# Optimization experiments

Hardware: AMD Instinct MI355X
Metric: run time of the kernel (lower is better)

Reference implementation:

```python
import jax, jax.numpy as jnp
import numpy as np

V = 50000      # vocab size
FEAT = 300     # glove dim
HID = 512      # num_hidden
C = 20         # class_num (GAT feature width)
L = 2          # num_layers
NH = 4         # num_heads
K = 3          # diffusion hops
ALPHA = 0.1    # teleport prob
N = 76800      # total nodes in batched graph
E = 1250000    # total edges
B = 512        # number of graphs (docs)
SLOPE = 0.2    # leaky relu slope (DGL GAT default)


def setup_inputs() -> dict:
    key = jax.random.key(0)
    ks = jax.random.split(key, 12)
    node_ids = jax.random.randint(ks[0], (N,), 0, V)
    edge_src = jax.random.randint(ks[1], (E,), 0, N)
    edge_dst = jax.random.randint(ks[2], (E,), 0, N)
    graph_ids = jnp.sort(jax.random.randint(ks[3], (N,), 0, B))
    emb = jax.random.uniform(ks[4], (V, FEAT), minval=-0.1, maxval=0.1, dtype=jnp.float32)
    W1 = jax.random.normal(ks[5], (FEAT, HID), dtype=jnp.float32) / np.sqrt(FEAT)
    b1 = jnp.zeros((HID,), jnp.float32)
    W2 = jax.random.normal(ks[6], (HID, C), dtype=jnp.float32) / np.sqrt(HID)
    b2 = jnp.zeros((C,), jnp.float32)
    gat_W = jax.random.normal(ks[7], (L, NH, C, C), dtype=jnp.float32) / np.sqrt(C)
    gat_asrc = jax.random.normal(ks[8], (L, NH, C), dtype=jnp.float32) * 0.1
    gat_adst = jax.random.normal(ks[9], (L, NH, C), dtype=jnp.float32) * 0.1
    ws_W = jax.random.normal(ks[10], (C, 1), dtype=jnp.float32) / np.sqrt(C)
    ws_b = jnp.zeros((1,), jnp.float32)
    return {"node_ids": node_ids, "edge_src": edge_src, "edge_dst": edge_dst,
            "graph_ids": graph_ids, "emb": emb, "W1": W1, "b1": b1, "W2": W2,
            "b2": b2, "gat_W": gat_W, "gat_asrc": gat_asrc, "gat_adst": gat_adst,
            "ws_W": ws_W, "ws_b": ws_b}


def _segment_softmax(e, dst, n):
    # e: [NH, E] edge scores; softmax over edges sharing the same destination node
    seg_max = jax.vmap(lambda v: jax.ops.segment_max(v, dst, num_segments=n))(e)
    seg_max = jnp.where(jnp.isfinite(seg_max), seg_max, 0.0)
    ex = jnp.exp(e - seg_max[:, dst])
    denom = jax.vmap(lambda v: jax.ops.segment_sum(v, dst, num_segments=n))(ex)
    return ex / (denom[:, dst] + 1e-9)


def _forward(node_ids, edge_src, edge_dst, graph_ids, emb, W1, b1, W2, b2,
             gat_W, gat_asrc, gat_adst, ws_W, ws_b):
    x = jnp.take(emb, node_ids, axis=0)              # [N, FEAT] embedding lookup
    x = jax.nn.relu(x @ W1 + b1)                     # [N, HID]
    h = x @ W2 + b2                                  # [N, C]
    for l in range(L):
        z = jnp.einsum('nc,hcd->hnd', h, gat_W[l])   # [NH, N, C]
        es = jnp.einsum('hnd,hd->hn', z, gat_asrc[l])
        ed = jnp.einsum('hnd,hd->hn', z, gat_adst[l])
        e = jax.nn.leaky_relu(es[:, edge_src] + ed[:, edge_dst], SLOPE)  # [NH, E]
        att = _segment_softmax(e, edge_dst, N)       # [NH, E]
        # attention diffusion: H <- (1-alpha) * A_att @ H + alpha * H0
        H0 = z
        Hc = z
        for _ in range(K):
            msg = att[:, :, None] * Hc[:, edge_src, :]                     # [NH, E, C]
            agg = jax.vmap(lambda m: jax.ops.segment_sum(m, edge_dst, num_segments=N))(msg)
            Hc = (1.0 - ALPHA) * agg + ALPHA * H0
        h = Hc.mean(axis=0)                          # merge='mean' over heads
        if l < L - 1:
            h = jax.nn.elu(h)
    gate = jax.nn.sigmoid(h @ ws_W + ws_b)           # [N, 1] WeightAndSum gate
    return jax.ops.segment_sum(h * gate, graph_ids, num_segments=B)  # [B, C]


def reference(node_ids, edge_src, edge_dst, graph_ids, emb, W1, b1, W2, b2,
              gat_W, gat_asrc, gat_adst, ws_W, ws_b):
    return _forward(node_ids, edge_src, edge_dst, graph_ids, emb, W1, b1, W2, b2,
                    gat_W, gat_asrc, gat_adst, ws_W, ws_b)
```

## Files before the change

kernel.cpp:

```cpp
#include <hip/hip_runtime.h>
#include <hip/hip_bf16.h>
#include <hip/hip_fp16.h>
#include <math.h>

#define VOCAB 50000
#define FEAT 300
#define KPAD 320
#define HID 512
#define C 20
#define NL 2
#define NH 4
#define KHOP 3
#define ALPHA 0.1f
#define NNODE 76800
#define NEDGE 1250000
#define NB 512
#define SLOPE 0.2f

#define NBKT 300
#define BKTCAP 5120
#define NSLOT (NBKT * BKTCAP)
#define EPB 5120
#define NEBLK ((NEDGE + EPB - 1) / EPB)

#define BM 32
#define VPAD 50048
#define SX_STRIDE 520
#define WSTRIDE 21

typedef float f32x4 __attribute__((ext_vector_type(4)));
typedef short bf16x8 __attribute__((ext_vector_type(8)));

__device__ inline unsigned short f2b(float x) {
  __hip_bfloat16 h = __float2bfloat16(x);
  return *reinterpret_cast<unsigned short*>(&h);
}

union R20 {
  struct { uint4 a, b; uint2 c; } v;
  __half2 h[10];
};
__device__ inline R20 ldrow20(const __half* p) {
  R20 r;
  r.v.a = *(const uint4*)p;
  r.v.b = *(const uint4*)(p + 8);
  r.v.c = *(const uint2*)(p + 16);
  return r;
}
__device__ inline void strow20(__half* p, const R20& r) {
  *(uint4*)p = r.v.a;
  *(uint4*)(p + 8) = r.v.b;
  *(uint2*)(p + 16) = r.v.c;
}

#define H2SWZ(v, pat) ({ union { __half2 h; int i; } _u; _u.h = (v);          \
                         _u.i = __builtin_amdgcn_ds_swizzle(_u.i, (pat));     \
                         _u.h; })
#define FSWZ(x, pat) __int_as_float(                                          \
    __builtin_amdgcn_ds_swizzle(__float_as_int(x), (pat)))
#define SLOTRED_H2(v) do {                                                    \
    v = __hadd2(v, H2SWZ(v, 0x101F));                                         \
    v = __hadd2(v, H2SWZ(v, 0x201F));                                         \
    v = __hadd2(v, H2SWZ(v, 0x401F)); } while (0)

__global__ void k_cvt_w1(const float* __restrict__ W1, ushort* __restrict__ W1t)
{
  int idx = blockIdx.x * 256 + threadIdx.x;
  int kc = idx >> 12;
  int rem = idx & 4095;
  int col = rem >> 3;
  int j = rem & 7;
  int k = kc * 8 + j;
  W1t[idx] = (k < FEAT) ? f2b(W1[(size_t)k * HID + col]) : (ushort)0;
}

__global__ void k_prep_coef(const float* __restrict__ gatW0,
                            const float* __restrict__ as0,
                            const float* __restrict__ ad0,
                            const float* __restrict__ b2,
                            float* __restrict__ coef, float* __restrict__ bb)
{
  int col = threadIdx.x;
  if (col >= 96) return;
  float cf[C];
  if (col < 80) {
    int hd = col / C, d = col - hd * C;
#pragma unroll
    for (int j = 0; j < C; j++) cf[j] = gatW0[(hd * C + j) * C + d];
  } else if (col < 88) {
    int hd = col - 80;
#pragma unroll
    for (int j = 0; j < C; j++) {
      float s = 0.f;
#pragma unroll
      for (int d = 0; d < C; d++) s += gatW0[(hd * C + j) * C + d] * as0[hd * C + d];
      cf[j] = s;
    }
  } else {
    int hd = col - 88;
#pragma unroll
    for (int j = 0; j < C; j++) {
      float s = 0.f;
#pragma unroll
      for (int d = 0; d < C; d++) s += gatW0[(hd * C + j) * C + d] * ad0[hd * C + d];
      cf[j] = s;
    }
  }
  float bbv = 0.f;
#pragma unroll
  for (int j = 0; j < C; j++) { coef[col * C + j] = cf[j]; bbv += b2[j] * cf[j]; }
  bb[col] = bbv;
}

__global__ void k_prep_wcp(const float* __restrict__ W2,
                           const float* __restrict__ coef,
                           ushort* __restrict__ Wcpt)
{
  int idx = blockIdx.x * 256 + threadIdx.x;
  int kc = idx / 768;
  int rem = idx - kc * 768;
  int col = rem >> 3;
  int j = rem & 7;
  int k = kc * 8 + j;
  float s = 0.f;
#pragma unroll
  for (int jj = 0; jj < C; jj++) s += W2[(size_t)k * C + jj] * coef[col * C + jj];
  Wcpt[idx] = f2b(s);
}

__global__ __launch_bounds__(512, 6) void k_mlp_mfma(
    const float* __restrict__ emb, const ushort* __restrict__ W1t,
    const float* __restrict__ b1, const ushort* __restrict__ Wcpt,
    const float* __restrict__ bb, __half* __restrict__ zfull,
    float* __restrict__ esf, float* __restrict__ edf)
{
  __shared__ ushort smem[16640];
  ushort* sA = smem;
  ushort* sX = smem;

  const int t = threadIdx.x;
  const int lane = t & 63;
  const int w = t >> 6;
  const int v0 = blockIdx.x * BM;
  const int l15 = lane & 15;
  const int l4 = lane >> 4;
  const int cb = w * 64;

#pragma unroll
  for (int j = 0; j < 3; j++) {
    int chunk = j * 512 + t;
    if (chunk < 1280) {
      int row = chunk & 31;
      int kc = chunk >> 5;
      int vr = v0 + row;
      if (vr >= VOCAB) vr = VOCAB - 1;
      int k0 = kc * 8;
      const float* p = emb + (size_t)vr * FEAT + k0;
      ushort u[8];
      if (k0 + 8 <= FEAT) {
        float4 x = *(const float4*)p;
        float4 y = *(const float4*)(p + 4);
        u[0] = f2b(x.x); u[1] = f2b(x.y); u[2] = f2b(x.z); u[3] = f2b(x.w);
        u[4] = f2b(y.x); u[5] = f2b(y.y); u[6] = f2b(y.z); u[7] = f2b(y.w);
      } else {
#pragma unroll
        for (int q = 0; q < 8; q++)
          u[q] = (k0 + q < FEAT) ? f2b(p[q]) : (ushort)0;
      }
      *(uint4*)(sA + (size_t)chunk * 8) = *(const uint4*)u;
    }
  }
  __syncthreads();

  f32x4 acc[2][4];
#pragma unroll
  for (int rt = 0; rt < 2; rt++)
#pragma unroll
    for (int ct = 0; ct < 4; ct++) acc[rt][ct] = (f32x4)0.f;

  for (int ks = 0; ks < 10; ks++) {
    const int kcb = ks * 4 + l4;
    bf16x8 a0 = *(const bf16x8*)(sA + ((size_t)kcb * 32 + l15) * 8);
    bf16x8 a1 = *(const bf16x8*)(sA + ((size_t)kcb * 32 + 16 + l15) * 8);
    const ushort* wb = W1t + ((size_t)kcb * 512 + cb + l15) * 8;
    bf16x8 bf[4];
#pragma unroll
    for (int ct = 0; ct < 4; ct++) bf[ct] = *(const bf16x8*)(wb + ct * 128);
#pragma unroll
    for (int ct = 0; ct < 4; ct++) {
      acc[0][ct] = __builtin_amdgcn_mfma_f32_16x16x32_bf16(a0, bf[ct], acc[0][ct], 0, 0, 0);
      acc[1][ct] = __builtin_amdgcn_mfma_f32_16x16x32_bf16(a1, bf[ct], acc[1][ct], 0, 0, 0);
    }
  }
  __syncthreads();

#pragma unroll
  for (int rt = 0; rt < 2; rt++)
#pragma unroll
    for (int ct = 0; ct < 4; ct++) {
      int col = cb + ct * 16 + l15;
      float bias = b1[col];
#pragma unroll
      for (int r4 = 0; r4 < 4; r4++) {
        int row = rt * 16 + l4 * 4 + r4;
        float x = fmaxf(acc[rt][ct][r4] + bias, 0.f);
        sX[(size_t)row * SX_STRIDE + col] = f2b(x);
      }
    }
  __syncthreads();

  const int ntile = (w < 4) ? 2 : 1;
  for (int i = 0; i < ntile; i++) {
    const int tt = (i == 0) ? w : 8 + w;
    const int rt = tt & 1, ct = tt >> 1;
    const ushort* xb = sX + (size_t)(rt * 16 + l15) * SX_STRIDE + l4 * 8;
    const ushort* wbp = Wcpt + ((size_t)l4 * 96 + ct * 16 + l15) * 8;
    bf16x8 bv[16];
#pragma unroll
    for (int ks = 0; ks < 16; ks++)
      bv[ks] = *(const bf16x8*)(wbp + (size_t)ks * 3072);
    f32x4 a2 = (f32x4)0.f;
#pragma unroll
    for (int ks = 0; ks < 16; ks++) {
      bf16x8 av = *(const bf16x8*)(xb + ks * 32);
      a2 = __builtin_amdgcn_mfma_f32_16x16x32_bf16(av, bv[ks], a2, 0, 0, 0);
    }
    const int col = ct * 16 + l15;
    const float bias = bb[col];
#pragma unroll
    for (int r = 0; r < 4; r++) {
      const int vrow = v0 + rt * 16 + l4 * 4 + r;
      if (vrow >= VOCAB) continue;
      float val = a2[r] + bias;
      if (col < 80) {
        int hd = col / C, c = col - hd * C;
        zfull[((size_t)vrow * NH + hd) * 20 + c] = __float2half_rn(val);
      } else if (col < 88) {
        esf[(size_t)vrow * NH + (col - 80)] = val;
      } else {
        edf[(size_t)vrow * NH + (col - 88)] = val;
      }
    }
  }
}

__global__ __launch_bounds__(256) void k_bkt_scatter(
    const int* __restrict__ src, const int* __restrict__ dst,
    int* __restrict__ gcur, int* __restrict__ gbuf)
{
  __shared__ int hist[NBKT];
  __shared__ int lcur[NBKT];
  const int t = threadIdx.x;
  for (int i = t; i < NBKT; i += 256) hist[i] = 0;
  __syncthreads();
  const int base = blockIdx.x * EPB;
#pragma unroll
  for (int j = 0; j < 20; j++) {
    int e = base + j * 256 + t;
    if (e < NEDGE) atomicAdd(&hist[dst[e] >> 8], 1);
  }
  __syncthreads();
  for (int i = t; i < NBKT; i += 256) {
    int v = hist[i];
    lcur[i] = v ? atomicAdd(&gcur[i], v) : 0;
  }
  __syncthreads();
#pragma unroll
  for (int j = 0; j < 20; j++) {
    int e = base + j * 256 + t;
    if (e < NEDGE) {
      int d = dst[e];
      int b = d >> 8;
      int idx = atomicAdd(&lcur[b], 1);
      if (idx < BKTCAP)
        gbuf[(size_t)b * BKTCAP + idx] = (src[e] << 8) | (d & 255);
    }
  }
}

__global__ __launch_bounds__(256) void k_csr_build(
    const int* __restrict__ gcur, const int* __restrict__ gbuf,
    const int* __restrict__ node_ids, int* __restrict__ offs,
    int* __restrict__ deg, int* __restrict__ srcc, int* __restrict__ srcv)
{
  __shared__ int shist[256];
  __shared__ int lcur[256];
  __shared__ int wsum[4];
  const int b = blockIdx.x;
  const int t = threadIdx.x;
  const int base = b * BKTCAP;
  int nb = gcur[b];
  if (nb > BKTCAP) nb = BKTCAP;
  shist[t] = 0;
  __syncthreads();
  for (int i = t; i < nb; i += 256)
    atomicAdd(&shist[gbuf[base + i] & 255], 1);
  __syncthreads();
  int v = shist[t];
  int x = v;
#pragma unroll
  for (int off = 1; off < 64; off <<= 1) {
    int y = __shfl_up(x, off, 64);
    if ((t & 63) >= off) x += y;
  }
  if ((t & 63) == 63) wsum[t >> 6] = x;
  __syncthreads();
  int waveoff = 0;
#pragma unroll
  for (int w = 0; w < 4; w++) waveoff += (w < (t >> 6)) ? wsum[w] : 0;
  int pre = base + waveoff + x - v;
  offs[b * 256 + t] = pre;
  deg[b * 256 + t] = v;
  lcur[t] = pre;
  __syncthreads();
  for (int i = t; i < nb; i += 256) {
    int p = gbuf[base + i];
    int slot = atomicAdd(&lcur[p & 255], 1);
    int s = p >> 8;
    srcc[slot] = s;
    srcv[slot] = node_ids[s];
  }
}

__global__ __launch_bounds__(256) void k_hop_first(
    const int* __restrict__ offs, const int* __restrict__ deg,
    const int* __restrict__ sidx,
    const float* __restrict__ esT, const float* __restrict__ edT,
    const int* __restrict__ ids, const __half* __restrict__ Zt,
    __half* __restrict__ att, float* __restrict__ invden,
    __half* __restrict__ Hout)
{
  const int t = threadIdx.x;
  const int head = t & 3;
  const int eslot = (t >> 2) & 7;
  const int n = blockIdx.x * 8 + (t >> 5);
  const int g = n * NH + head;
  const int idn = ids ? ids[n] : n;
  const int beg = offs[n], end = beg + deg[n];
  const float edv = edT[(size_t)idn * NH + head];
  R20 h0 = ldrow20(Zt + ((size_t)idn * NH + head) * 20);
  __half2 agg[10];
#pragma unroll
  for (int q = 0; q < 10; q++) agg[q] = __floats2half2_rn(0.f, 0.f);
  float den = 0.f;
  int p = beg + eslot;
  while (p + 8 < end) {
    int sv0 = sidx[p];
    int sv1 = sidx[p + 8];
    float es0 = esT[(size_t)sv0 * NH + head];
    float es1 = esT[(size_t)sv1 * NH + head];
    R20 r0 = ldrow20(Zt + ((size_t)sv0 * NH + head) * 20);
    R20 r1 = ldrow20(Zt + ((size_t)sv1 * NH + head) * 20);
    float e0 = es0 + edv; e0 = e0 > 0.f ? e0 : SLOPE * e0;
    float e1 = es1 + edv; e1 = e1 > 0.f ? e1 : SLOPE * e1;
    float ex0 = __expf(e0), ex1 = __expf(e1);
    att[(size_t)p * NH + head] = __float2half_rn(ex0);
    att[(size_t)(p + 8) * NH + head] = __float2half_rn(ex1);
    den += ex0 + ex1;
    __half2 a0 = __float2half2_rn(ex0);
    __half2 a1 = __float2half2_rn(ex1);
#pragma unroll
    for (int q = 0; q < 10; q++) {
      agg[q] = __hfma2(a0, r0.h[q], agg[q]);
      agg[q] = __hfma2(a1, r1.h[q], agg[q]);
    }
    p += 16;
  }
  if (p < end) {
    int sv0 = sidx[p];
    float es0 = esT[(size_t)sv0 * NH + head];
    R20 r0 = ldrow20(Zt + ((size_t)sv0 * NH + head) * 20);
    float e0 = es0 + edv; e0 = e0 > 0.f ? e0 : SLOPE * e0;
    float ex0 = __expf(e0);
    att[(size_t)p * NH + head] = __float2half_rn(ex0);
    den += ex0;
    __half2 a0 = __float2half2_rn(ex0);
#pragma unroll
    for (int q = 0; q < 10; q++) agg[q] = __hfma2(a0, r0.h[q], agg[q]);
  }
#pragma unroll
  for (int q = 0; q < 10; q++) SLOTRED_H2(agg[q]);
  den += FSWZ(den, 0x101F);
  den += FSWZ(den, 0x201F);
  den += FSWZ(den, 0x401F);
  if (eslot == 0) {
    float inv = 1.f / (den + 1e-9f);
    invden[g] = inv;
    __half2 s2 = __float2half2_rn(inv * (1.0f - ALPHA));
    __half2 al = __float2half2_rn(ALPHA);
    R20 o;
#pragma unroll
    for (int q = 0; q < 10; q++)
      o.h[q] = __hfma2(s2, agg[q], __hmul2(al, h0.h[q]));
    strow20(Hout + (size_t)g * 20, o);
  }
}

__global__ __launch_bounds__(256) void k_hop_mid(
    const int* __restrict__ offs, const int* __restrict__ deg,
    const int* __restrict__ srcc,
    const __half* __restrict__ att, const float* __restrict__ invden,
    const __half* __restrict__ Hin, const __half* __restrict__ Zt,
    const int* __restrict__ ids, __half* __restrict__ Hout)
{
  const int t = threadIdx.x;
  const int head = t & 3;
  const int eslot = (t >> 2) & 7;
  const int n = blockIdx.x * 8 + (t >> 5);
  const int g = n * NH + head;
  const int idn = ids ? ids[n] : n;
  const int beg = offs[n], end = beg + deg[n];
  R20 h0 = ldrow20(Zt + ((size_t)idn * NH + head) * 20);
  __half2 agg[10];
#pragma unroll
  for (int q = 0; q < 10; q++) agg[q] = __floats2half2_rn(0.f, 0.f);
  int p = beg + eslot;
  while (p + 8 < end) {
    __half a0h = att[(size_t)p * NH + head];
    __half a1h = att[(size_t)(p + 8) * NH + head];
    int sn0 = srcc[p];
    int sn1 = srcc[p + 8];
    R20 r0 = ldrow20(Hin + ((size_t)sn0 * NH + head) * 20);
    R20 r1 = ldrow20(Hin + ((size_t)sn1 * NH + head) * 20);
    __half2 a0 = __half2half2(a0h);
    __half2 a1 = __half2half2(a1h);
#pragma unroll
    for (int q = 0; q < 10; q++) {
      agg[q] = __hfma2(a0, r0.h[q], agg[q]);
      agg[q] = __hfma2(a1, r1.h[q], agg[q]);
    }
    p += 16;
  }
  if (p < end) {
    __half a0h = att[(size_t)p * NH + head];
    int sn0 = srcc[p];
    R20 r0 = ldrow20(Hin + ((size_t)sn0 * NH + head) * 20);
    __half2 a0 = __half2half2(a0h);
#pragma unroll
    for (int q = 0; q < 10; q++) agg[q] = __hfma2(a0, r0.h[q], agg[q]);
  }
#pragma unroll
  for (int q = 0; q < 10; q++) SLOTRED_H2(agg[q]);
  if (eslot == 0) {
    __half2 s2 = __float2half2_rn(invden[g] * (1.0f - ALPHA));
    __half2 al = __float2half2_rn(ALPHA);
    R20 o;
#pragma unroll
    for (int q = 0; q < 10; q++)
      o.h[q] = __hfma2(s2, agg[q], __hmul2(al, h0.h[q]));
    strow20(Hout + (size_t)g * 20, o);
  }
}

__global__ __launch_bounds__(256) void k_hop_last_proj(
    const int* __restrict__ offs, const int* __restrict__ deg,
    const int* __restrict__ srcc,
    const __half* __restrict__ att, const float* __restrict__ invden,
    const __half* __restrict__ Hin, const __half* __restrict__ Zt,
    const int* __restrict__ ids,
    const float* __restrict__ gatW1, const float* __restrict__ as1,
    const float* __restrict__ ad1,
    __half* __restrict__ zb, float* __restrict__ es, float* __restrict__ ed)
{
  __shared__ float sWt[NH * C * WSTRIDE];
  __shared__ float sa[NH * C], sd[NH * C];
  const int t = threadIdx.x;
  for (int i = t; i < NH * C * C; i += 256) {
    int h = i / (C * C);
    int r = i - h * C * C;
    int c = r / C;
    int d = r - c * C;
    sWt[(h * C + d) * WSTRIDE + c] = gatW1[i];
  }
  if (t < NH * C) { sa[t] = as1[t]; sd[t] = ad1[t]; }
  __syncthreads();

  const int head = t & 3;
  const int eslot = (t >> 2) & 7;
  const int n = blockIdx.x * 8 + (t >> 5);
  const int g = n * NH + head;
  const int idn = ids ? ids[n] : n;
  const int beg = offs[n], end = beg + deg[n];
  R20 h0 = ldrow20(Zt + ((size_t)idn * NH + head) * 20);
  __half2 agg[10];
#pragma unroll
  for (int q = 0; q < 10; q++) agg[q] = __floats2half2_rn(0.f, 0.f);
  int p = beg + eslot;
  while (p + 8 < end) {
    __half a0h = att[(size_t)p * NH + head];
    __half a1h = att[(size_t)(p + 8) * NH + head];
    int sn0 = srcc[p];
    int sn1 = srcc[p + 8];
    R20 r0 = ldrow20(Hin + ((size_t)sn0 * NH + head) * 20);
    R20 r1 = ldrow20(Hin + ((size_t)sn1 * NH + head) * 20);
    __half2 a0 = __half2half2(a0h);
    __half2 a1 = __half2half2(a1h);
#pragma unroll
    for (int q = 0; q < 10; q++) {
      agg[q] = __hfma2(a0, r0.h[q], agg[q]);
      agg[q] = __hfma2(a1, r1.h[q], agg[q]);
    }
    p += 16;
  }
  if (p < end) {
    __half a0h = att[(size_t)p * NH + head];
    int sn0 = srcc[p];
    R20 r0 = ldrow20(Hin + ((size_t)sn0 * NH + head) * 20);
    __half2 a0 = __half2half2(a0h);
#pragma unroll
    for (int q = 0; q < 10; q++) agg[q] = __hfma2(a0, r0.h[q], agg[q]);
  }
#pragma unroll
  for (int q = 0; q < 10; q++) SLOTRED_H2(agg[q]);

  __half2 s2 = __float2half2_rn(invden[g] * (1.0f - ALPHA));
  __half2 al = __float2half2_rn(ALPHA);
  float o[C];
#pragma unroll
  for (int q = 0; q < 10; q++) {
    __half2 m = __hfma2(s2, agg[q], __hmul2(al, h0.h[q]));
    m = __hadd2(m, H2SWZ(m, 0x041F));
    m = __hadd2(m, H2SWZ(m, 0x081F));
    float2 f = __half22float2(m);
    float v0 = f.x * 0.25f, v1 = f.y * 0.25f;
    o[2 * q]     = v0 > 0.f ? v0 : __expf(v0) - 1.f;
    o[2 * q + 1] = v1 > 0.f ? v1 : __expf(v1) - 1.f;
  }

  float esp = 0.f, edp = 0.f;
#pragma unroll
  for (int j = 0; j < 3; j++) {
    int d = eslot + j * 8;
    if (d < C) {
      const float* wrow = &sWt[(head * C + d) * WSTRIDE];
      float zv = 0.f;
#pragma unroll
      for (int c = 0; c < C; c++) zv += o[c] * wrow[c];
      esp += zv * sa[head * C + d];
      edp += zv * sd[head * C + d];
      zb[((size_t)n * NH + head) * 20 + d] = __float2half_rn(zv);
    }
  }
  esp += FSWZ(esp, 0x101F);
  esp += FSWZ(esp, 0x201F);
  esp += FSWZ(esp, 0x401F);
  edp += FSWZ(edp, 0x101F);
  edp += FSWZ(edp, 0x201F);
  edp += FSWZ(edp, 0x401F);
  if (eslot == 0) {
    es[g] = esp;
    ed[g] = edp;
  }
}

#define RSPAN 16
__global__ __launch_bounds__(256) void k_hop_last_final(
    const int* __restrict__ offs, const int* __restrict__ deg,
    const int* __restrict__ srcc,
    const __half* __restrict__ att, const float* __restrict__ invden,
    const __half* __restrict__ Hin, const __half* __restrict__ Zt,
    const int* __restrict__ gids, const float* __restrict__ wsW,
    const float* __restrict__ wsb, float* __restrict__ out)
{
  __shared__ float sacc[RSPAN * C];
  __shared__ int sgmin;
  const int t = threadIdx.x;
  const int head = t & 3;
  const int eslot = (t >> 2) & 7;
  const int n = blockIdx.x * 8 + (t >> 5);
  const int g = n * NH + head;
  const int beg = offs[n], end = beg + deg[n];
  for (int i = t; i < RSPAN * C; i += 256) sacc[i] = 0.f;
  if (t == 0) sgmin = gids[blockIdx.x * 8];
  __syncthreads();
  R20 h0 = ldrow20(Zt + ((size_t)n * NH + head) * 20);
  __half2 agg[10];
#pragma unroll
  for (int q = 0; q < 10; q++) agg[q] = __floats2half2_rn(0.f, 0.f);
  int p = beg + eslot;
  while (p + 8 < end) {
    __half a0h = att[(size_t)p * NH + head];
    __half a1h = att[(size_t)(p + 8) * NH + head];
    int sn0 = srcc[p];
    int sn1 = srcc[p + 8];
    R20 r0 = ldrow20(Hin + ((size_t)sn0 * NH + head) * 20);
    R20 r1 = ldrow20(Hin + ((size_t)sn1 * NH + head) * 20);
    __half2 a0 = __half2half2(a0h);
    __half2 a1 = __half2half2(a1h);
#pragma unroll
    for (int q = 0; q < 10; q++) {
      agg[q] = __hfma2(a0, r0.h[q], agg[q]);
      agg[q] = __hfma2(a1, r1.h[q], agg[q]);
    }
    p += 16;
  }
  if (p < end) {
    __half a0h = att[(size_t)p * NH + head];
    int sn0 = srcc[p];
    R20 r0 = ldrow20(Hin + ((size_t)sn0 * NH + head) * 20);
    __half2 a0 = __half2half2(a0h);
#pragma unroll
    for (int q = 0; q < 10; q++) agg[q] = __hfma2(a0, r0.h[q], agg[q]);
  }
#pragma unroll
  for (int q = 0; q < 10; q++) SLOTRED_H2(agg[q]);
  if (eslot == 0) {
    __half2 s2 = __float2half2_rn(invden[g] * (1.0f - ALPHA));
    __half2 al = __float2half2_rn(ALPHA);
    float o[C];
#pragma unroll
    for (int q = 0; q < 10; q++) {
      __half2 m = __hfma2(s2, agg[q], __hmul2(al, h0.h[q]));
      m = __hadd2(m, H2SWZ(m, 0x041F));
      m = __hadd2(m, H2SWZ(m, 0x081F));
      float2 f = __half22float2(m);
      o[2 * q]     = f.x * 0.25f;
      o[2 * q + 1] = f.y * 0.25f;
    }
    float dotp = 0.f;
#pragma unroll
    for (int j = 0; j < 5; j++) {
      int c = head * 5 + j;
      dotp += o[c] * wsW[c];
    }
    dotp += FSWZ(dotp, 0x041F);
    dotp += FSWZ(dotp, 0x081F);
    const float gate = 1.f / (1.f + __expf(-(dotp + wsb[0])));
    const int b = gids[n];
    const int lb = b - sgmin;
    if (lb < RSPAN) {
#pragma unroll
      for (int j = 0; j < 5; j++) {
        int c = head * 5 + j;
        atomicAdd(&sacc[lb * C + c], o[c] * gate);
      }
    } else {
#pragma unroll
      for (int j = 0; j < 5; j++) {
        int c = head * 5 + j;
        atomicAdd(&out[(size_t)b * C + c], o[c] * gate);
      }
    }
  }
  __syncthreads();
  for (int i = t; i < RSPAN * C; i += 256) {
    float v = sacc[i];
    if (v != 0.f) atomicAdd(&out[(size_t)(sgmin + i / C) * C + (i - (i / C) * C)], v);
  }
}

extern "C" void kernel_launch(void* const* d_in, const int* in_sizes, int n_in,
                              void* d_out, int out_size, void* d_ws, size_t ws_size,
                              hipStream_t stream)
{
  const int*   node_ids = (const int*)  d_in[0];
  const int*   edge_src = (const int*)  d_in[1];
  const int*   edge_dst = (const int*)  d_in[2];
  const int*   graph_ids= (const int*)  d_in[3];
  const float* emb      = (const float*)d_in[4];
  const float* W1       = (const float*)d_in[5];
  const float* b1       = (const float*)d_in[6];
  const float* W2       = (const float*)d_in[7];
  const float* b2       = (const float*)d_in[8];
  const float* gat_W    = (const float*)d_in[9];
  const float* gat_asrc = (const float*)d_in[10];
  const float* gat_adst = (const float*)d_in[11];
  const float* ws_W     = (const float*)d_in[12];
  const float* ws_b     = (const float*)d_in[13];
  float* out = (float*)d_out;

  float* esf    = (float*)d_ws;
  float* edf    = esf   + (size_t)VPAD * NH;
  float* es     = edf   + (size_t)VPAD * NH;
  float* ed     = es    + (size_t)NNODE * NH;
  float* invden = ed    + (size_t)NNODE * NH;
  float* bb     = invden+ (size_t)NNODE * NH;
  float* coef   = bb + 96;
  int*   offs   = (int*)(coef + 96 * C);
  int*   deg    = offs + NNODE;
  int*   gcur   = deg + NNODE;
  int*   srcc   = gcur + NBKT;
  int*   srcv   = srcc + NSLOT;
  uintptr_t a16 = ((uintptr_t)(srcv + NSLOT) + 15) & ~(uintptr_t)15;
  __half* zfull = (__half*)a16;
  __half* zb    = zfull + (size_t)VPAD * NH * 20;
  __half* bufA  = zb    + (size_t)NNODE * NH * 20;
  __half* bufB  = bufA  + (size_t)NNODE * NH * 20;
  ushort* W1t   = (ushort*)(bufB + (size_t)NNODE * NH * 20);
  ushort* Wcpt  = W1t + (size_t)40 * 512 * 8;
  uintptr_t x16 = ((uintptr_t)(Wcpt + 64 * 96 * 8) + 15) & ~(uintptr_t)15;
  int*    gbuf  = (int*)x16;
  __half* att   = (__half*)x16;

  hipMemsetAsync(out, 0, (size_t)NB * C * sizeof(float), stream);
  hipMemsetAsync(gcur, 0, NBKT * sizeof(int), stream);

  k_cvt_w1<<<(40 * 512 * 8) / 256, 256, 0, stream>>>(W1, W1t);
  k_prep_coef<<<1, 128, 0, stream>>>(gat_W, gat_asrc, gat_adst, b2, coef, bb);
  k_prep_wcp<<<(64 * 96 * 8) / 256, 256, 0, stream>>>(W2, coef, Wcpt);

  k_bkt_scatter<<<NEBLK, 256, 0, stream>>>(edge_src, edge_dst, gcur, gbuf);
  k_csr_build<<<NBKT, 256, 0, stream>>>(gcur, gbuf, node_ids,
                                        offs, deg, srcc, srcv);

  k_mlp_mfma<<<VPAD / BM, 512, 0, stream>>>(emb, W1t, b1, Wcpt, bb,
                                            zfull, esf, edf);

  const int HB = NNODE / 8;
  k_hop_first<<<HB, 256, 0, stream>>>(offs, deg, srcv, esf, edf, node_ids,
                                      zfull, att, invden, bufA);
  k_hop_mid<<<HB, 256, 0, stream>>>(offs, deg, srcc, att, invden, bufA, zfull,
                                    node_ids, bufB);
  k_hop_last_proj<<<HB, 256, 0, stream>>>(offs, deg, srcc, att, invden, bufB,
                                          zfull, node_ids,
                                          gat_W + (size_t)NH * C * C,
                                          gat_asrc + NH * C, gat_adst + NH * C,
                                          zb, es, ed);
  k_hop_first<<<HB, 256, 0, stream>>>(offs, deg, srcc, es, ed,
                                      (const int*)nullptr, zb, att, invden,
                                      bufA);
  k_hop_mid<<<HB, 256, 0, stream>>>(offs, deg, srcc, att, invden, bufA, zb,
                                    (const int*)nullptr, bufB);
  k_hop_last_final<<<HB, 256, 0, stream>>>(offs, deg, srcc, att, invden, bufB,
                                           zb, graph_ids, ws_W, ws_b, out);
}
```

Baseline: 398.3 us.

## Pad feature rows to 24 halves and pack attention scores into row

Node feature rows grow from 20 to 24 halves so each row is three aligned 16-byte loads, and the per-node source/destination attention scores are stored as fp16 in the padding slots. Edge gathers now fetch the score together with the feature row instead of from separate float arrays. The MLP kernel also gets explicit double-buffered weight loads and a lower occupancy hint. The trade-off is 20% more bytes per row in the gathered buffers and reduced precision for the attention scores.

```diff
diff --git a/kernel.cpp b/kernel.cpp
--- a/kernel.cpp
+++ b/kernel.cpp
@@ -27,6 +27,7 @@
 #define VPAD 50048
 #define SX_STRIDE 520
 #define WSTRIDE 21
+#define RW 24
 
 typedef float f32x4 __attribute__((ext_vector_type(4)));
 typedef short bf16x8 __attribute__((ext_vector_type(8)));
@@ -36,21 +37,22 @@
   return *reinterpret_cast<unsigned short*>(&h);
 }
 
-union R20 {
-  struct { uint4 a, b; uint2 c; } v;
-  __half2 h[10];
+union R24 {
+  uint4 u[3];
+  __half2 h[12];
+  __half s[24];
 };
-__device__ inline R20 ldrow20(const __half* p) {
-  R20 r;
-  r.v.a = *(const uint4*)p;
-  r.v.b = *(const uint4*)(p + 8);
-  r.v.c = *(const uint2*)(p + 16);
+__device__ inline R24 ldrow24(const __half* p) {
+  R24 r;
+  r.u[0] = *(const uint4*)p;
+  r.u[1] = *(const uint4*)(p + 8);
+  r.u[2] = *(const uint4*)(p + 16);
   return r;
 }
-__device__ inline void strow20(__half* p, const R20& r) {
-  *(uint4*)p = r.v.a;
-  *(uint4*)(p + 8) = r.v.b;
-  *(uint2*)(p + 16) = r.v.c;
+__device__ inline void strow24(__half* p, const R24& r) {
+  *(uint4*)p = r.u[0];
+  *(uint4*)(p + 8) = r.u[1];
+  *(uint4*)(p + 16) = r.u[2];
 }
 
 #define H2SWZ(v, pat) ({ union { __half2 h; int i; } _u; _u.h = (v);          \
@@ -128,11 +130,10 @@
   Wcpt[idx] = f2b(s);
 }
 
-__global__ __launch_bounds__(512, 6) void k_mlp_mfma(
+__global__ __launch_bounds__(512, 4) void k_mlp_mfma(
     const float* __restrict__ emb, const ushort* __restrict__ W1t,
     const float* __restrict__ b1, const ushort* __restrict__ Wcpt,
-    const float* __restrict__ bb, __half* __restrict__ zfull,
-    float* __restrict__ esf, float* __restrict__ edf)
+    const float* __restrict__ bb, __half* __restrict__ zfull)
 {
   __shared__ ushort smem[16640];
   ushort* sA = smem;
@@ -178,19 +179,31 @@
 #pragma unroll
     for (int ct = 0; ct < 4; ct++) acc[rt][ct] = (f32x4)0.f;
 
-  for (int ks = 0; ks < 10; ks++) {
-    const int kcb = ks * 4 + l4;
-    bf16x8 a0 = *(const bf16x8*)(sA + ((size_t)kcb * 32 + l15) * 8);
-    bf16x8 a1 = *(const bf16x8*)(sA + ((size_t)kcb * 32 + 16 + l15) * 8);
-    const ushort* wb = W1t + ((size_t)kcb * 512 + cb + l15) * 8;
-    bf16x8 bf[4];
-#pragma unroll
-    for (int ct = 0; ct < 4; ct++) bf[ct] = *(const bf16x8*)(wb + ct * 128);
-#pragma unroll
-    for (int ct = 0; ct < 4; ct++) {
-      acc[0][ct] = __builtin_amdgcn_mfma_f32_16x16x32_bf16(a0, bf[ct], acc[0][ct], 0, 0, 0);
-      acc[1][ct] = __builtin_amdgcn_mfma_f32_16x16x32_bf16(a1, bf[ct], acc[1][ct], 0, 0, 0);
-    }
+  const ushort* wbase = W1t + ((size_t)l4 * 512 + cb + l15) * 8;
+  bf16x8 bfA[4], bfB[4];
+#define LOADB(DST, KS)                                                        \
+  { _Pragma("unroll")                                                         \
+    for (int ct = 0; ct < 4; ct++)                                            \
+      DST[ct] = *(const bf16x8*)(wbase + (size_t)(KS) * 16384 + ct * 128); }
+#define DOMFMA(BF, KS)                                                        \
+  { const int kcb = (KS) * 4 + l4;                                            \
+    bf16x8 a0 = *(const bf16x8*)(sA + ((size_t)kcb * 32 + l15) * 8);          \
+    bf16x8 a1 = *(const bf16x8*)(sA + ((size_t)kcb * 32 + 16 + l15) * 8);     \
+    _Pragma("unroll")                                                         \
+    for (int ct = 0; ct < 4; ct++) {                                          \
+      acc[0][ct] = __builtin_amdgcn_mfma_f32_16x16x32_bf16(a0, BF[ct],        \
+                                                           acc[0][ct], 0, 0, 0);\
+      acc[1][ct] = __builtin_amdgcn_mfma_f32_16x16x32_bf16(a1, BF[ct],        \
+                                                           acc[1][ct], 0, 0, 0);\
+    } }
+
+  LOADB(bfA, 0);
+#pragma unroll
+  for (int ks2 = 0; ks2 < 10; ks2 += 2) {
+    LOADB(bfB, ks2 + 1);
+    DOMFMA(bfA, ks2);
+    if (ks2 + 2 < 10) LOADB(bfA, ks2 + 2);
+    DOMFMA(bfB, ks2 + 1);
   }
   __syncthreads();
 
@@ -234,11 +247,11 @@
       float val = a2[r] + bias;
       if (col < 80) {
         int hd = col / C, c = col - hd * C;
-        zfull[((size_t)vrow * NH + hd) * 20 + c] = __float2half_rn(val);
+        zfull[((size_t)vrow * NH + hd) * RW + c] = __float2half_rn(val);
       } else if (col < 88) {
-        esf[(size_t)vrow * NH + (col - 80)] = val;
+        zfull[((size_t)vrow * NH + (col - 80)) * RW + 20] = __float2half_rn(val);
       } else {
-        edf[(size_t)vrow * NH + (col - 88)] = val;
+        zfull[((size_t)vrow * NH + (col - 88)) * RW + 21] = __float2half_rn(val);
       }
     }
   }
@@ -325,7 +338,6 @@
 __global__ __launch_bounds__(256) void k_hop_first(
     const int* __restrict__ offs, const int* __restrict__ deg,
     const int* __restrict__ sidx,
-    const float* __restrict__ esT, const float* __restrict__ edT,
     const int* __restrict__ ids, const __half* __restrict__ Zt,
     __half* __restrict__ att, float* __restrict__ invden,
     __half* __restrict__ Hout)
@@ -337,8 +349,8 @@
   const int g = n * NH + head;
   const int idn = ids ? ids[n] : n;
   const int beg = offs[n], end = beg + deg[n];
-  const float edv = edT[(size_t)idn * NH + head];
-  R20 h0 = ldrow20(Zt + ((size_t)idn * NH + head) * 20);
+  R24 h0 = ldrow24(Zt + ((size_t)idn * NH + head) * RW);
+  const float edv = __half2float(h0.s[21]);
   __half2 agg[10];
 #pragma unroll
   for (int q = 0; q < 10; q++) agg[q] = __floats2half2_rn(0.f, 0.f);
@@ -347,12 +359,10 @@
   while (p + 8 < end) {
     int sv0 = sidx[p];
     int sv1 = sidx[p + 8];
-    float es0 = esT[(size_t)sv0 * NH + head];
-    float es1 = esT[(size_t)sv1 * NH + head];
-    R20 r0 = ldrow20(Zt + ((size_t)sv0 * NH + head) * 20);
-    R20 r1 = ldrow20(Zt + ((size_t)sv1 * NH + head) * 20);
-    float e0 = es0 + edv; e0 = e0 > 0.f ? e0 : SLOPE * e0;
-    float e1 = es1 + edv; e1 = e1 > 0.f ? e1 : SLOPE * e1;
+    R24 r0 = ldrow24(Zt + ((size_t)sv0 * NH + head) * RW);
+    R24 r1 = ldrow24(Zt + ((size_t)sv1 * NH + head) * RW);
+    float e0 = __half2float(r0.s[20]) + edv; e0 = e0 > 0.f ? e0 : SLOPE * e0;
+    float e1 = __half2float(r1.s[20]) + edv; e1 = e1 > 0.f ? e1 : SLOPE * e1;
     float ex0 = __expf(e0), ex1 = __expf(e1);
     att[(size_t)p * NH + head] = __float2half_rn(ex0);
     att[(size_t)(p + 8) * NH + head] = __float2half_rn(ex1);
@@ -368,9 +378,8 @@
   }
   if (p < end) {
     int sv0 = sidx[p];
-    float es0 = esT[(size_t)sv0 * NH + head];
-    R20 r0 = ldrow20(Zt + ((size_t)sv0 * NH + head) * 20);
-    float e0 = es0 + edv; e0 = e0 > 0.f ? e0 : SLOPE * e0;
+    R24 r0 = ldrow24(Zt + ((size_t)sv0 * NH + head) * RW);
+    float e0 = __half2float(r0.s[20]) + edv; e0 = e0 > 0.f ? e0 : SLOPE * e0;
     float ex0 = __expf(e0);
     att[(size_t)p * NH + head] = __float2half_rn(ex0);
     den += ex0;
@@ -388,11 +397,13 @@
     invden[g] = inv;
     __half2 s2 = __float2half2_rn(inv * (1.0f - ALPHA));
     __half2 al = __float2half2_rn(ALPHA);
-    R20 o;
+    R24 o;
 #pragma unroll
     for (int q = 0; q < 10; q++)
       o.h[q] = __hfma2(s2, agg[q], __hmul2(al, h0.h[q]));
-    strow20(Hout + (size_t)g * 20, o);
+    o.h[10] = __floats2half2_rn(0.f, 0.f);
+    o.h[11] = o.h[10];
+    strow24(Hout + (size_t)g * RW, o);
   }
 }
 
@@ -410,7 +421,7 @@
   const int g = n * NH + head;
   const int idn = ids ? ids[n] : n;
   const int beg = offs[n], end = beg + deg[n];
-  R20 h0 = ldrow20(Zt + ((size_t)idn * NH + head) * 20);
+  R24 h0 = ldrow24(Zt + ((size_t)idn * NH + head) * RW);
   __half2 agg[10];
 #pragma unroll
   for (int q = 0; q < 10; q++) agg[q] = __floats2half2_rn(0.f, 0.f);
@@ -420,8 +431,8 @@
     __half a1h = att[(size_t)(p + 8) * NH + head];
     int sn0 = srcc[p];
     int sn1 = srcc[p + 8];
-    R20 r0 = ldrow20(Hin + ((size_t)sn0 * NH + head) * 20);
-    R20 r1 = ldrow20(Hin + ((size_t)sn1 * NH + head) * 20);
+    R24 r0 = ldrow24(Hin + ((size_t)sn0 * NH + head) * RW);
+    R24 r1 = ldrow24(Hin + ((size_t)sn1 * NH + head) * RW);
     __half2 a0 = __half2half2(a0h);
     __half2 a1 = __half2half2(a1h);
 #pragma unroll
@@ -434,7 +445,7 @@
   if (p < end) {
     __half a0h = att[(size_t)p * NH + head];
     int sn0 = srcc[p];
-    R20 r0 = ldrow20(Hin + ((size_t)sn0 * NH + head) * 20);
+    R24 r0 = ldrow24(Hin + ((size_t)sn0 * NH + head) * RW);
     __half2 a0 = __half2half2(a0h);
 #pragma unroll
     for (int q = 0; q < 10; q++) agg[q] = __hfma2(a0, r0.h[q], agg[q]);
@@ -444,11 +455,13 @@
   if (eslot == 0) {
     __half2 s2 = __float2half2_rn(invden[g] * (1.0f - ALPHA));
     __half2 al = __float2half2_rn(ALPHA);
-    R20 o;
+    R24 o;
 #pragma unroll
     for (int q = 0; q < 10; q++)
       o.h[q] = __hfma2(s2, agg[q], __hmul2(al, h0.h[q]));
-    strow20(Hout + (size_t)g * 20, o);
+    o.h[10] = __floats2half2_rn(0.f, 0.f);
+    o.h[11] = o.h[10];
+    strow24(Hout + (size_t)g * RW, o);
   }
 }
 
@@ -459,8 +472,7 @@
     const __half* __restrict__ Hin, const __half* __restrict__ Zt,
     const int* __restrict__ ids,
     const float* __restrict__ gatW1, const float* __restrict__ as1,
-    const float* __restrict__ ad1,
-    __half* __restrict__ zb, float* __restrict__ es, float* __restrict__ ed)
+    const float* __restrict__ ad1, __half* __restrict__ zb)
 {
   __shared__ float sWt[NH * C * WSTRIDE];
   __shared__ float sa[NH * C], sd[NH * C];
@@ -481,7 +493,7 @@
   const int g = n * NH + head;
   const int idn = ids ? ids[n] : n;
   const int beg = offs[n], end = beg + deg[n];
-  R20 h0 = ldrow20(Zt + ((size_t)idn * NH + head) * 20);
+  R24 h0 = ldrow24(Zt + ((size_t)idn * NH + head) * RW);
   __half2 agg[10];
 #pragma unroll
   for (int q = 0; q < 10; q++) agg[q] = __floats2half2_rn(0.f, 0.f);
@@ -491,8 +503,8 @@
     __half a1h = att[(size_t)(p + 8) * NH + head];
     int sn0 = srcc[p];
     int sn1 = srcc[p + 8];
-    R20 r0 = ldrow20(Hin + ((size_t)sn0 * NH + head) * 20);
-    R20 r1 = ldrow20(Hin + ((size_t)sn1 * NH + head) * 20);
+    R24 r0 = ldrow24(Hin + ((size_t)sn0 * NH + head) * RW);
+    R24 r1 = ldrow24(Hin + ((size_t)sn1 * NH + head) * RW);
     __half2 a0 = __half2half2(a0h);
     __half2 a1 = __half2half2(a1h);
 #pragma unroll
@@ -505,7 +517,7 @@
   if (p < end) {
     __half a0h = att[(size_t)p * NH + head];
     int sn0 = srcc[p];
-    R20 r0 = ldrow20(Hin + ((size_t)sn0 * NH + head) * 20);
+    R24 r0 = ldrow24(Hin + ((size_t)sn0 * NH + head) * RW);
     __half2 a0 = __half2half2(a0h);
 #pragma unroll
     for (int q = 0; q < 10; q++) agg[q] = __hfma2(a0, r0.h[q], agg[q]);
@@ -528,6 +540,7 @@
   }
 
   float esp = 0.f, edp = 0.f;
+  __half* zrow = zb + ((size_t)n * NH + head) * RW;
 #pragma unroll
   for (int j = 0; j < 3; j++) {
     int d = eslot + j * 8;
@@ -538,7 +551,7 @@
       for (int c = 0; c < C; c++) zv += o[c] * wrow[c];
       esp += zv * sa[head * C + d];
       edp += zv * sd[head * C + d];
-      zb[((size_t)n * NH + head) * 20 + d] = __float2half_rn(zv);
+      zrow[d] = __float2half_rn(zv);
     }
   }
   esp += FSWZ(esp, 0x101F);
@@ -548,8 +561,8 @@
   edp += FSWZ(edp, 0x201F);
   edp += FSWZ(edp, 0x401F);
   if (eslot == 0) {
-    es[g] = esp;
-    ed[g] = edp;
+    zrow[20] = __float2half_rn(esp);
+    zrow[21] = __float2half_rn(edp);
   }
 }
 
@@ -573,7 +586,7 @@
   for (int i = t; i < RSPAN * C; i += 256) sacc[i] = 0.f;
   if (t == 0) sgmin = gids[blockIdx.x * 8];
   __syncthreads();
-  R20 h0 = ldrow20(Zt + ((size_t)n * NH + head) * 20);
+  R24 h0 = ldrow24(Zt + ((size_t)n * NH + head) * RW);
   __half2 agg[10];
 #pragma unroll
   for (int q = 0; q < 10; q++) agg[q] = __floats2half2_rn(0.f, 0.f);
@@ -583,8 +596,8 @@
     __half a1h = att[(size_t)(p + 8) * NH + head];
     int sn0 = srcc[p];
     int sn1 = srcc[p + 8];
-    R20 r0 = ldrow20(Hin + ((size_t)sn0 * NH + head) * 20);
-    R20 r1 = ldrow20(Hin + ((size_t)sn1 * NH + head) * 20);
+    R24 r0 = ldrow24(Hin + ((size_t)sn0 * NH + head) * RW);
+    R24 r1 = ldrow24(Hin + ((size_t)sn1 * NH + head) * RW);
     __half2 a0 = __half2half2(a0h);
     __half2 a1 = __half2half2(a1h);
 #pragma unroll
@@ -597,7 +610,7 @@
   if (p < end) {
     __half a0h = att[(size_t)p * NH + head];
     int sn0 = srcc[p];
-    R20 r0 = ldrow20(Hin + ((size_t)sn0 * NH + head) * 20);
+    R24 r0 = ldrow24(Hin + ((size_t)sn0 * NH + head) * RW);
     __half2 a0 = __half2half2(a0h);
 #pragma unroll
     for (int q = 0; q < 10; q++) agg[q] = __hfma2(a0, r0.h[q], agg[q]);
@@ -669,12 +682,8 @@
   const float* ws_b     = (const float*)d_in[13];
   float* out = (float*)d_out;
 
-  float* esf    = (float*)d_ws;
-  float* edf    = esf   + (size_t)VPAD * NH;
-  float* es     = edf   + (size_t)VPAD * NH;
-  float* ed     = es    + (size_t)NNODE * NH;
-  float* invden = ed    + (size_t)NNODE * NH;
-  float* bb     = invden+ (size_t)NNODE * NH;
+  float* invden = (float*)d_ws;
+  float* bb     = invden + (size_t)NNODE * NH;
   float* coef   = bb + 96;
   int*   offs   = (int*)(coef + 96 * C);
   int*   deg    = offs + NNODE;
@@ -683,10 +692,10 @@
   int*   srcv   = srcc + NSLOT;
   uintptr_t a16 = ((uintptr_t)(srcv + NSLOT) + 15) & ~(uintptr_t)15;
   __half* zfull = (__half*)a16;
-  __half* zb    = zfull + (size_t)VPAD * NH * 20;
-  __half* bufA  = zb    + (size_t)NNODE * NH * 20;
-  __half* bufB  = bufA  + (size_t)NNODE * NH * 20;
-  ushort* W1t   = (ushort*)(bufB + (size_t)NNODE * NH * 20);
+  __half* zb    = zfull + (size_t)VPAD * NH * RW;
+  __half* bufA  = zb    + (size_t)NNODE * NH * RW;
+  __half* bufB  = bufA  + (size_t)NNODE * NH * RW;
+  ushort* W1t   = (ushort*)(bufB + (size_t)NNODE * NH * RW);
   ushort* Wcpt  = W1t + (size_t)40 * 512 * 8;
   uintptr_t x16 = ((uintptr_t)(Wcpt + 64 * 96 * 8) + 15) & ~(uintptr_t)15;
   int*    gbuf  = (int*)x16;
@@ -703,11 +712,10 @@
   k_csr_build<<<NBKT, 256, 0, stream>>>(gcur, gbuf, node_ids,
                                         offs, deg, srcc, srcv);
 
-  k_mlp_mfma<<<VPAD / BM, 512, 0, stream>>>(emb, W1t, b1, Wcpt, bb,
-                                            zfull, esf, edf);
+  k_mlp_mfma<<<VPAD / BM, 512, 0, stream>>>(emb, W1t, b1, Wcpt, bb, zfull);
 
   const int HB = NNODE / 8;
-  k_hop_first<<<HB, 256, 0, stream>>>(offs, deg, srcv, esf, edf, node_ids,
+  k_hop_first<<<HB, 256, 0, stream>>>(offs, deg, srcv, node_ids,
                                       zfull, att, invden, bufA);
   k_hop_mid<<<HB, 256, 0, stream>>>(offs, deg, srcc, att, invden, bufA, zfull,
                                     node_ids, bufB);
@@ -715,10 +723,9 @@
                                           zfull, node_ids,
                                           gat_W + (size_t)NH * C * C,
                                           gat_asrc + NH * C, gat_adst + NH * C,
-                                          zb, es, ed);
-  k_hop_first<<<HB, 256, 0, stream>>>(offs, deg, srcc, es, ed,
-                                      (const int*)nullptr, zb, att, invden,
-                                      bufA);
+                                          zb);
+  k_hop_first<<<HB, 256, 0, stream>>>(offs, deg, srcc, (const int*)nullptr,
+                                      zb, att, invden, bufA);
   k_hop_mid<<<HB, 256, 0, stream>>>(offs, deg, srcc, att, invden, bufA, zb,
                                     (const int*)nullptr, bufB);
   k_hop_last_final<<<HB, 256, 0, stream>>>(offs, deg, srcc, att, invden, bufB,
```

Result: slower. 419.9 us (+5.4%).
